# Performance work log

Measured on AMD Instinct MI355X. Metric: run time of the kernel, lower is better.

The kernel has to match this reference:

```python
import jax, jax.numpy as jnp
import numpy as np

N = 100000
K = 16
C_IN = 64
C_MID = 64   # max(in_channels, out_channels // 2)
C_OUT = 128
EPS = 1e-5


def setup_inputs() -> dict:
    key = jax.random.key(0)
    ks = jax.random.split(key, 4)
    feat = jax.random.normal(ks[0], (N, C_IN), dtype=jnp.float32)
    reference_index = jax.random.randint(ks[1], (N, K), 0, N, dtype=jnp.int64)
    # Kaiming-ish init for the two Linear layers (torch Linear default scale)
    W1 = jax.random.normal(ks[2], (C_IN, C_MID), dtype=jnp.float32) / np.sqrt(C_IN)
    W2 = jax.random.normal(ks[3], (C_MID, C_OUT), dtype=jnp.float32) / np.sqrt(C_MID)
    return {
        "feat": feat,
        "reference_index": reference_index,
        "W1": W1,
        "b1": jnp.zeros((C_MID,), jnp.float32),
        "gamma1": jnp.ones((C_MID,), jnp.float32),
        "beta1": jnp.zeros((C_MID,), jnp.float32),
        "W2": W2,
        "b2": jnp.zeros((C_OUT,), jnp.float32),
        "gamma2": jnp.ones((C_OUT,), jnp.float32),
        "beta2": jnp.zeros((C_OUT,), jnp.float32),
    }


def _bn(x, gamma, beta):
    # BatchNorm1d in training mode: biased batch stats over the row dim.
    mean = jnp.mean(x, axis=0)
    var = jnp.var(x, axis=0)
    return (x - mean) * jax.lax.rsqrt(var + EPS) * gamma + beta


def reference(feat, reference_index, W1, b1, gamma1, beta1, W2, b2, gamma2, beta2):
    # grouping (with_xyz=False): gather neighbor features -> [N, K, C_IN]
    grouped = feat[reference_index]
    x = grouped.reshape(-1, C_IN)                 # [N*K, C_IN]
    h = jax.nn.relu(_bn(x @ W1 + b1, gamma1, beta1))   # [N*K, C_MID]
    h = jax.nn.relu(_bn(h @ W2 + b2, gamma2, beta2))   # [N*K, C_OUT]
    out = h.reshape(N, K, C_OUT).max(axis=1)      # max-pool over neighbors
    return out
```

## Files before the change

### kernel.cpp

```cpp
#include <hip/hip_runtime.h>
#include <hip/hip_bf16.h>

#define N_PTS 100000
#define KNN   16
#define NK    (N_PTS * KNN)
#define CIN   64
#define CMID  64
#define COUT  128

#define HSLC    64
#define SEG_CNT 25000
#define SEG_U32 12500

#define OFF_Z2B   0
#define OFF_Z1B   25600000
#define OFF_CNT   38400000
#define OFF_STATS 38800000
#define OFF_W2BF  38801536
#define OFF_W1BF  38817920

typedef __attribute__((ext_vector_type(8))) short bf16x8;
typedef __attribute__((ext_vector_type(4))) float f32x4;
union U8 { uint4 u; bf16x8 v; unsigned short s[8]; };

__device__ __forceinline__ unsigned short f2bf(float f) {
    unsigned u = __float_as_uint(f);
    unsigned r = (u + 0x7fffu + ((u >> 16) & 1u)) >> 16;
    return (unsigned short)r;
}

__global__ __launch_bounds__(256) void hist_k(const int* __restrict__ idx,
                                              unsigned short* __restrict__ pc) {
    __shared__ unsigned int smem[SEG_U32];
    int seg  = blockIdx.x & 3;
    int slc  = blockIdx.x >> 2;
    int base = seg * SEG_CNT;

    for (int i = threadIdx.x; i < SEG_U32; i += 256) smem[i] = 0;
    __syncthreads();

    const int4* ip = (const int4*)idx;
    const int per = NK / 4 / HSLC;
    int s = slc * per, e = s + per;
    for (int i = s + threadIdx.x; i < e; i += 256) {
        int4 v = ip[i];
        int a;
        a = v.x - base; if ((unsigned)a < (unsigned)SEG_CNT)
            atomicAdd(&smem[a >> 1], 1u << ((a & 1) * 16));
        a = v.y - base; if ((unsigned)a < (unsigned)SEG_CNT)
            atomicAdd(&smem[a >> 1], 1u << ((a & 1) * 16));
        a = v.z - base; if ((unsigned)a < (unsigned)SEG_CNT)
            atomicAdd(&smem[a >> 1], 1u << ((a & 1) * 16));
        a = v.w - base; if ((unsigned)a < (unsigned)SEG_CNT)
            atomicAdd(&smem[a >> 1], 1u << ((a & 1) * 16));
    }
    __syncthreads();

    unsigned int* outp = (unsigned int*)(pc + (size_t)slc * N_PTS) + seg * SEG_U32;
    for (int i = threadIdx.x; i < SEG_U32; i += 256) outp[i] = smem[i];
}

__global__ __launch_bounds__(256) void sum_counts_k(const unsigned short* __restrict__ pc,
                                                    float* __restrict__ counts,
                                                    const float* __restrict__ W2,
                                                    unsigned short* __restrict__ w2bf,
                                                    const float* __restrict__ W1,
                                                    unsigned short* __restrict__ w1bf) {
    if (blockIdx.x == 196) {
        for (int e = threadIdx.x; e < 8192; e += 256) {
            int j = e & 7, lane = (e >> 3) & 63, kh = (e >> 9) & 1, nt = e >> 10;
            int k = kh * 32 + (lane >> 4) * 8 + j;
            int n = nt * 16 + (lane & 15);
            w2bf[e] = f2bf(W2[k * COUT + n]);
        }
        return;
    }
    if (blockIdx.x == 197) {
        for (int e = threadIdx.x; e < 4096; e += 256) {
            int j = e & 7, lane = (e >> 3) & 63, kh = (e >> 9) & 1, nt = e >> 10;
            int k = kh * 32 + (lane >> 4) * 8 + j;
            int n = nt * 16 + (lane & 15);
            w1bf[e] = f2bf(W1[k * CMID + n]);
        }
        return;
    }
    int i = blockIdx.x * 256 + threadIdx.x;
    if (i >= N_PTS / 2) return;
    const unsigned int* p = (const unsigned int*)pc;
    unsigned int u = 0;
    #pragma unroll
    for (int s = 0; s < HSLC; s++) u += p[s * (N_PTS / 2) + i];
    float2 r;
    r.x = (float)(u & 0xffffu);
    r.y = (float)(u >> 16);
    ((float2*)counts)[i] = r;
}

__global__ __launch_bounds__(256) void gemm1_k(const float* __restrict__ feat,
                                               const unsigned short* __restrict__ w1bf,
                                               const float* __restrict__ b1,
                                               const float* __restrict__ counts,
                                               unsigned short* __restrict__ z1b,
                                               float* __restrict__ S1,
                                               float* __restrict__ Q1) {
    int lane = threadIdx.x & 63, wid = threadIdx.x >> 6;
    int il = lane & 15, quad = lane >> 4;

    bf16x8 wf[4][2];
    const uint4* wp = (const uint4*)w1bf;
    #pragma unroll
    for (int nt = 0; nt < 4; nt++) {
        U8 t0; t0.u = wp[(nt * 2 + 0) * 64 + lane]; wf[nt][0] = t0.v;
        U8 t1; t1.u = wp[(nt * 2 + 1) * 64 + lane]; wf[nt][1] = t1.v;
    }
    float bias[4];
    #pragma unroll
    for (int nt = 0; nt < 4; nt++) bias[nt] = b1[nt * 16 + il];

    float s[4] = {0, 0, 0, 0}, q[4] = {0, 0, 0, 0};

    int wgid = blockIdx.x * 4 + wid;
    for (int tile = wgid; tile < N_PTS / 16; tile += gridDim.x * 4) {
        int m0 = tile * 16;
        const float* fr = feat + (size_t)(m0 + il) * 64;
        float4 fa = *(const float4*)(fr + quad * 8);
        float4 fb = *(const float4*)(fr + quad * 8 + 4);
        float4 fc = *(const float4*)(fr + 32 + quad * 8);
        float4 fd = *(const float4*)(fr + 32 + quad * 8 + 4);
        U8 ua, ub;
        ua.s[0] = f2bf(fa.x); ua.s[1] = f2bf(fa.y); ua.s[2] = f2bf(fa.z); ua.s[3] = f2bf(fa.w);
        ua.s[4] = f2bf(fb.x); ua.s[5] = f2bf(fb.y); ua.s[6] = f2bf(fb.z); ua.s[7] = f2bf(fb.w);
        ub.s[0] = f2bf(fc.x); ub.s[1] = f2bf(fc.y); ub.s[2] = f2bf(fc.z); ub.s[3] = f2bf(fc.w);
        ub.s[4] = f2bf(fd.x); ub.s[5] = f2bf(fd.y); ub.s[6] = f2bf(fd.z); ub.s[7] = f2bf(fd.w);

        float4 cnt4 = *(const float4*)(counts + m0 + quad * 4);
        #pragma unroll
        for (int nt = 0; nt < 4; nt++) {
            f32x4 acc = {bias[nt], bias[nt], bias[nt], bias[nt]};
            acc = __builtin_amdgcn_mfma_f32_16x16x32_bf16(ua.v, wf[nt][0], acc, 0, 0, 0);
            acc = __builtin_amdgcn_mfma_f32_16x16x32_bf16(ub.v, wf[nt][1], acc, 0, 0, 0);
            unsigned short* zp = z1b + (size_t)(m0 + quad * 4) * 64 + nt * 16 + il;
            zp[0]   = f2bf(acc[0]);
            zp[64]  = f2bf(acc[1]);
            zp[128] = f2bf(acc[2]);
            zp[192] = f2bf(acc[3]);
            s[nt] += cnt4.x * acc[0] + cnt4.y * acc[1] + cnt4.z * acc[2] + cnt4.w * acc[3];
            q[nt] += cnt4.x * acc[0] * acc[0] + cnt4.y * acc[1] * acc[1]
                   + cnt4.z * acc[2] * acc[2] + cnt4.w * acc[3] * acc[3];
        }
    }
    #pragma unroll
    for (int m = 16; m <= 32; m <<= 1) {
        #pragma unroll
        for (int nt = 0; nt < 4; nt++) {
            s[nt] += __shfl_xor(s[nt], m, 64);
            q[nt] += __shfl_xor(q[nt], m, 64);
        }
    }
    __shared__ float sred[2][4][4][16];
    if (quad == 0) {
        #pragma unroll
        for (int nt = 0; nt < 4; nt++) { sred[0][wid][nt][il] = s[nt]; sred[1][wid][nt][il] = q[nt]; }
    }
    __syncthreads();
    if (threadIdx.x < 128) {
        int which = threadIdx.x >> 6, c = threadIdx.x & 63;
        float t = sred[which][0][c >> 4][c & 15] + sred[which][1][c >> 4][c & 15]
                + sred[which][2][c >> 4][c & 15] + sred[which][3][c >> 4][c & 15];
        atomicAdd(which ? &Q1[c] : &S1[c], t);
    }
}

__device__ __forceinline__ bf16x8 bnrelu(uint4 r, float4 alo, float4 ahi,
                                         float4 blo, float4 bhi) {
    float z0 = __uint_as_float(r.x << 16), z1 = __uint_as_float(r.x & 0xffff0000u);
    float z2 = __uint_as_float(r.y << 16), z3 = __uint_as_float(r.y & 0xffff0000u);
    float z4 = __uint_as_float(r.z << 16), z5 = __uint_as_float(r.z & 0xffff0000u);
    float z6 = __uint_as_float(r.w << 16), z7 = __uint_as_float(r.w & 0xffff0000u);
    U8 o;
    o.s[0] = f2bf(fmaxf(fmaf(alo.x, z0, blo.x), 0.f));
    o.s[1] = f2bf(fmaxf(fmaf(alo.y, z1, blo.y), 0.f));
    o.s[2] = f2bf(fmaxf(fmaf(alo.z, z2, blo.z), 0.f));
    o.s[3] = f2bf(fmaxf(fmaf(alo.w, z3, blo.w), 0.f));
    o.s[4] = f2bf(fmaxf(fmaf(ahi.x, z4, bhi.x), 0.f));
    o.s[5] = f2bf(fmaxf(fmaf(ahi.y, z5, bhi.y), 0.f));
    o.s[6] = f2bf(fmaxf(fmaf(ahi.z, z6, bhi.z), 0.f));
    o.s[7] = f2bf(fmaxf(fmaf(ahi.w, z7, bhi.w), 0.f));
    return o.v;
}

__global__ __launch_bounds__(256) void gemm2_k(const unsigned short* __restrict__ z1b,
                                               const unsigned short* __restrict__ w2bf,
                                               const float* __restrict__ S1,
                                               const float* __restrict__ Q1,
                                               const float* __restrict__ g1,
                                               const float* __restrict__ be1,
                                               const float* __restrict__ b2,
                                               const float* __restrict__ counts,
                                               unsigned short* __restrict__ z2b,
                                               float* __restrict__ S2,
                                               float* __restrict__ Q2) {
    __shared__ float Al[64], Bl[64];
    if (threadIdx.x < 64) {
        const float inv = 1.0f / (float)NK;
        float m = S1[threadIdx.x] * inv;
        float v = Q1[threadIdx.x] * inv - m * m;
        float a = g1[threadIdx.x] * rsqrtf(v + 1e-5f);
        Al[threadIdx.x] = a;
        Bl[threadIdx.x] = be1[threadIdx.x] - m * a;
    }
    __syncthreads();

    int lane = threadIdx.x & 63, wid = threadIdx.x >> 6;
    int il = lane & 15, quad = lane >> 4;

    float4 a0lo = *(const float4*)(Al + quad * 8);
    float4 a0hi = *(const float4*)(Al + quad * 8 + 4);
    float4 b0lo = *(const float4*)(Bl + quad * 8);
    float4 b0hi = *(const float4*)(Bl + quad * 8 + 4);
    float4 a1lo = *(const float4*)(Al + 32 + quad * 8);
    float4 a1hi = *(const float4*)(Al + 32 + quad * 8 + 4);
    float4 b1lo = *(const float4*)(Bl + 32 + quad * 8);
    float4 b1hi = *(const float4*)(Bl + 32 + quad * 8 + 4);

    bf16x8 bfr[8][2];
    const uint4* wp = (const uint4*)w2bf;
    #pragma unroll
    for (int nt = 0; nt < 8; nt++) {
        U8 t0; t0.u = wp[(nt * 2 + 0) * 64 + lane]; bfr[nt][0] = t0.v;
        U8 t1; t1.u = wp[(nt * 2 + 1) * 64 + lane]; bfr[nt][1] = t1.v;
    }
    float bias[8];
    #pragma unroll
    for (int nt = 0; nt < 8; nt++) bias[nt] = b2[nt * 16 + il];

    float s[8], q[8];
    #pragma unroll
    for (int j = 0; j < 8; j++) { s[j] = 0.f; q[j] = 0.f; }

    int wgid = blockIdx.x * 4 + wid;
    for (int tile = wgid; tile < N_PTS / 16; tile += gridDim.x * 4) {
        int m0 = tile * 16;
        const uint4* ar = (const uint4*)(z1b + (size_t)(m0 + il) * 64);
        uint4 ra0 = ar[quad];
        uint4 ra1 = ar[4 + quad];
        bf16x8 af0 = bnrelu(ra0, a0lo, a0hi, b0lo, b0hi);
        bf16x8 af1 = bnrelu(ra1, a1lo, a1hi, b1lo, b1hi);
        float4 cnt4 = *(const float4*)(counts + m0 + quad * 4);
        #pragma unroll
        for (int nt = 0; nt < 8; nt++) {
            f32x4 acc = {bias[nt], bias[nt], bias[nt], bias[nt]};
            acc = __builtin_amdgcn_mfma_f32_16x16x32_bf16(af0, bfr[nt][0], acc, 0, 0, 0);
            acc = __builtin_amdgcn_mfma_f32_16x16x32_bf16(af1, bfr[nt][1], acc, 0, 0, 0);
            unsigned short* zp = z2b + ((size_t)(nt >> 2) * N_PTS + m0 + quad * 4) * 64
                                     + (nt & 3) * 16 + il;
            zp[0]   = f2bf(acc[0]);
            zp[64]  = f2bf(acc[1]);
            zp[128] = f2bf(acc[2]);
            zp[192] = f2bf(acc[3]);
            s[nt] += cnt4.x * acc[0] + cnt4.y * acc[1] + cnt4.z * acc[2] + cnt4.w * acc[3];
            q[nt] += cnt4.x * acc[0] * acc[0] + cnt4.y * acc[1] * acc[1]
                   + cnt4.z * acc[2] * acc[2] + cnt4.w * acc[3] * acc[3];
        }
    }
    #pragma unroll
    for (int m = 16; m <= 32; m <<= 1) {
        #pragma unroll
        for (int nt = 0; nt < 8; nt++) {
            s[nt] += __shfl_xor(s[nt], m, 64);
            q[nt] += __shfl_xor(q[nt], m, 64);
        }
    }
    __shared__ float sred[2][4][8][16];
    if (quad == 0) {
        #pragma unroll
        for (int nt = 0; nt < 8; nt++) { sred[0][wid][nt][il] = s[nt]; sred[1][wid][nt][il] = q[nt]; }
    }
    __syncthreads();
    {
        int which = threadIdx.x >> 7, c = threadIdx.x & 127;
        float t = sred[which][0][c >> 4][c & 15] + sred[which][1][c >> 4][c & 15]
                + sred[which][2][c >> 4][c & 15] + sred[which][3][c >> 4][c & 15];
        atomicAdd(which ? &Q2[c] : &S2[c], t);
    }
}

__global__ __launch_bounds__(256) void gather_k(const unsigned int* __restrict__ z2u,
                                                const int* __restrict__ idx,
                                                const float* __restrict__ S2,
                                                const float* __restrict__ Q2,
                                                const float* __restrict__ g2,
                                                const float* __restrict__ be2,
                                                float* __restrict__ out) {
    int lane = threadIdx.x & 63, wid = threadIdx.x >> 6;
    int half = blockIdx.x / (N_PTS / 8);
    int n    = (blockIdx.x % (N_PTS / 8)) * 8 + wid * 2 + (lane >> 5);
    int sl   = lane & 31;

    const float inv = 1.0f / (float)NK;
    float2 Sv = ((const float2*)S2)[half * 32 + sl];
    float2 Qv = ((const float2*)Q2)[half * 32 + sl];
    float2 gv = ((const float2*)g2)[half * 32 + sl];
    float2 bv = ((const float2*)be2)[half * 32 + sl];
    float m0c = Sv.x * inv, m1c = Sv.y * inv;
    float a0 = gv.x * rsqrtf(Qv.x * inv - m0c * m0c + 1e-5f);
    float a1 = gv.y * rsqrtf(Qv.y * inv - m1c * m1c + 1e-5f);
    float b0 = bv.x - m0c * a0;
    float b1 = bv.y - m1c * a1;

    const int* ip = idx + n * KNN;
    const unsigned int* zh = z2u + (size_t)half * N_PTS * 32;
    float mx0 = -1e30f, mn0 = 1e30f, mx1 = -1e30f, mn1 = 1e30f;
    #pragma unroll
    for (int k = 0; k < KNN; k++) {
        int j = ip[k];
        unsigned v = zh[(size_t)j * 32 + sl];
        float f0 = __uint_as_float(v << 16);
        float f1 = __uint_as_float(v & 0xffff0000u);
        mx0 = fmaxf(mx0, f0); mn0 = fminf(mn0, f0);
        mx1 = fmaxf(mx1, f1); mn1 = fminf(mn1, f1);
    }
    float2 r;
    r.x = fmaxf(fmaxf(fmaf(a0, mx0, b0), fmaf(a0, mn0, b0)), 0.f);
    r.y = fmaxf(fmaxf(fmaf(a1, mx1, b1), fmaf(a1, mn1, b1)), 0.f);
    ((float2*)(out + (size_t)n * COUT + half * 64))[sl] = r;
}

extern "C" void kernel_launch(void* const* d_in, const int* in_sizes, int n_in,
                              void* d_out, int out_size, void* d_ws, size_t ws_size,
                              hipStream_t stream) {
    const float* feat = (const float*)d_in[0];
    const int*   idx  = (const int*)d_in[1];
    const float* W1   = (const float*)d_in[2];
    const float* b1   = (const float*)d_in[3];
    const float* g1   = (const float*)d_in[4];
    const float* be1  = (const float*)d_in[5];
    const float* W2   = (const float*)d_in[6];
    const float* b2   = (const float*)d_in[7];
    const float* g2   = (const float*)d_in[8];
    const float* be2  = (const float*)d_in[9];
    float* out = (float*)d_out;

    char* ws = (char*)d_ws;
    unsigned short* z2b = (unsigned short*)(ws + OFF_Z2B);
    unsigned short* pc  = (unsigned short*)(ws + OFF_Z2B);
    unsigned short* z1b = (unsigned short*)(ws + OFF_Z1B);
    float* counts = (float*)(ws + OFF_CNT);
    float* S1 = (float*)(ws + OFF_STATS);
    float* Q1 = S1 + 64;
    float* S2 = S1 + 128;
    float* Q2 = S1 + 256;
    unsigned short* w2bf = (unsigned short*)(ws + OFF_W2BF);
    unsigned short* w1bf = (unsigned short*)(ws + OFF_W1BF);

    hipMemsetAsync(ws + OFF_STATS, 0, 1536, stream);

    hist_k<<<4 * HSLC, 256, 0, stream>>>(idx, pc);
    sum_counts_k<<<198, 256, 0, stream>>>(pc, counts, W2, w2bf, W1, w1bf);
    gemm1_k<<<512, 256, 0, stream>>>(feat, w1bf, b1, counts, z1b, S1, Q1);
    gemm2_k<<<512, 256, 0, stream>>>(z1b, w2bf, S1, Q1, g1, be1, b2, counts, z2b, S2, Q2);
    gather_k<<<2 * (N_PTS / 8), 256, 0, stream>>>((const unsigned int*)z2b, idx,
                                                  S2, Q2, g2, be2, out);
}
```

Baseline: 206.8 us.

## Switch intermediates to fp16, fold gamma sign into W2, packed-max gather

Intermediates and MFMA inputs move from bf16 to fp16, with packed round-toward-zero conversions. The MFMA operands are swapped so each lane writes four contiguous channels as one 8-byte store instead of four scattered 2-byte stores. The sign of gamma2 is folded into W2 and b2, so the gather only needs a max, which it does with v_pk_max_f16 instead of tracking both max and min in fp32. This cuts gather ALU work and speeds the GEMM stores, at the cost of fp16 range and precision risk and more stats registers.

```diff
diff --git a/kernel.cpp b/kernel.cpp
--- a/kernel.cpp
+++ b/kernel.cpp
@@ -12,21 +12,25 @@
 #define SEG_CNT 25000
 #define SEG_U32 12500
 
-#define OFF_Z2B   0
-#define OFF_Z1B   25600000
+#define OFF_Z2H   0
+#define OFF_Z1H   25600000
 #define OFF_CNT   38400000
 #define OFF_STATS 38800000
-#define OFF_W2BF  38801536
-#define OFF_W1BF  38817920
-
-typedef __attribute__((ext_vector_type(8))) short bf16x8;
+#define OFF_W2F   38801536
+#define OFF_W1F   38817920
+
+typedef __attribute__((ext_vector_type(8))) _Float16 f16x8;
+typedef __attribute__((ext_vector_type(2))) __fp16 fp16x2;
 typedef __attribute__((ext_vector_type(4))) float f32x4;
-union U8 { uint4 u; bf16x8 v; unsigned short s[8]; };
-
-__device__ __forceinline__ unsigned short f2bf(float f) {
-    unsigned u = __float_as_uint(f);
-    unsigned r = (u + 0x7fffu + ((u >> 16) & 1u)) >> 16;
-    return (unsigned short)r;
+union F8 { uint4 u; f16x8 v; };
+union PK { fp16x2 v; unsigned u; };
+union UH { unsigned u; _Float16 h[2]; };
+
+__device__ __forceinline__ unsigned pk2(float a, float b) {
+    PK p; p.v = __builtin_amdgcn_cvt_pkrtz(a, b); return p.u;
+}
+__device__ __forceinline__ unsigned pkmax(unsigned a, unsigned b) {
+    unsigned d; asm("v_pk_max_f16 %0, %1, %2" : "=v"(d) : "v"(a), "v"(b)); return d;
 }
 
 __global__ __launch_bounds__(256) void hist_k(const int* __restrict__ idx,
@@ -63,24 +67,25 @@
 __global__ __launch_bounds__(256) void sum_counts_k(const unsigned short* __restrict__ pc,
                                                     float* __restrict__ counts,
                                                     const float* __restrict__ W2,
-                                                    unsigned short* __restrict__ w2bf,
+                                                    const float* __restrict__ g2,
+                                                    _Float16* __restrict__ w2f,
                                                     const float* __restrict__ W1,
-                                                    unsigned short* __restrict__ w1bf) {
+                                                    _Float16* __restrict__ w1f) {
     if (blockIdx.x == 196) {
         for (int e = threadIdx.x; e < 8192; e += 256) {
-            int j = e & 7, lane = (e >> 3) & 63, kh = (e >> 9) & 1, nt = e >> 10;
+            int j = e & 7, lane = (e >> 3) & 63, kh = (e >> 9) & 1, cht = e >> 10;
             int k = kh * 32 + (lane >> 4) * 8 + j;
-            int n = nt * 16 + (lane & 15);
-            w2bf[e] = f2bf(W2[k * COUT + n]);
+            int n = cht * 16 + (lane & 15);
+            w2f[e] = (_Float16)(__builtin_copysignf(1.f, g2[n]) * W2[k * COUT + n]);
         }
         return;
     }
     if (blockIdx.x == 197) {
         for (int e = threadIdx.x; e < 4096; e += 256) {
-            int j = e & 7, lane = (e >> 3) & 63, kh = (e >> 9) & 1, nt = e >> 10;
+            int j = e & 7, lane = (e >> 3) & 63, kh = (e >> 9) & 1, cht = e >> 10;
             int k = kh * 32 + (lane >> 4) * 8 + j;
-            int n = nt * 16 + (lane & 15);
-            w1bf[e] = f2bf(W1[k * CMID + n]);
+            int n = cht * 16 + (lane & 15);
+            w1f[e] = (_Float16)(W1[k * CMID + n]);
         }
         return;
     }
@@ -97,27 +102,31 @@
 }
 
 __global__ __launch_bounds__(256) void gemm1_k(const float* __restrict__ feat,
-                                               const unsigned short* __restrict__ w1bf,
+                                               const _Float16* __restrict__ w1f,
                                                const float* __restrict__ b1,
                                                const float* __restrict__ counts,
-                                               unsigned short* __restrict__ z1b,
+                                               _Float16* __restrict__ z1h,
                                                float* __restrict__ S1,
                                                float* __restrict__ Q1) {
     int lane = threadIdx.x & 63, wid = threadIdx.x >> 6;
     int il = lane & 15, quad = lane >> 4;
 
-    bf16x8 wf[4][2];
-    const uint4* wp = (const uint4*)w1bf;
-    #pragma unroll
-    for (int nt = 0; nt < 4; nt++) {
-        U8 t0; t0.u = wp[(nt * 2 + 0) * 64 + lane]; wf[nt][0] = t0.v;
-        U8 t1; t1.u = wp[(nt * 2 + 1) * 64 + lane]; wf[nt][1] = t1.v;
-    }
-    float bias[4];
-    #pragma unroll
-    for (int nt = 0; nt < 4; nt++) bias[nt] = b1[nt * 16 + il];
-
-    float s[4] = {0, 0, 0, 0}, q[4] = {0, 0, 0, 0};
+    f16x8 wf[4][2];
+    const uint4* wp = (const uint4*)w1f;
+    #pragma unroll
+    for (int cht = 0; cht < 4; cht++) {
+        F8 t0; t0.u = wp[(cht * 2 + 0) * 64 + lane]; wf[cht][0] = t0.v;
+        F8 t1; t1.u = wp[(cht * 2 + 1) * 64 + lane]; wf[cht][1] = t1.v;
+    }
+    float4 bias[4];
+    #pragma unroll
+    for (int cht = 0; cht < 4; cht++) bias[cht] = *(const float4*)(b1 + cht * 16 + quad * 4);
+
+    float s[4][4], q[4][4];
+    #pragma unroll
+    for (int c = 0; c < 4; c++)
+        #pragma unroll
+        for (int r = 0; r < 4; r++) { s[c][r] = 0.f; q[c][r] = 0.f; }
 
     int wgid = blockIdx.x * 4 + wid;
     for (int tile = wgid; tile < N_PTS / 16; tile += gridDim.x * 4) {
@@ -127,80 +136,85 @@
         float4 fb = *(const float4*)(fr + quad * 8 + 4);
         float4 fc = *(const float4*)(fr + 32 + quad * 8);
         float4 fd = *(const float4*)(fr + 32 + quad * 8 + 4);
-        U8 ua, ub;
-        ua.s[0] = f2bf(fa.x); ua.s[1] = f2bf(fa.y); ua.s[2] = f2bf(fa.z); ua.s[3] = f2bf(fa.w);
-        ua.s[4] = f2bf(fb.x); ua.s[5] = f2bf(fb.y); ua.s[6] = f2bf(fb.z); ua.s[7] = f2bf(fb.w);
-        ub.s[0] = f2bf(fc.x); ub.s[1] = f2bf(fc.y); ub.s[2] = f2bf(fc.z); ub.s[3] = f2bf(fc.w);
-        ub.s[4] = f2bf(fd.x); ub.s[5] = f2bf(fd.y); ub.s[6] = f2bf(fd.z); ub.s[7] = f2bf(fd.w);
-
-        float4 cnt4 = *(const float4*)(counts + m0 + quad * 4);
-        #pragma unroll
-        for (int nt = 0; nt < 4; nt++) {
-            f32x4 acc = {bias[nt], bias[nt], bias[nt], bias[nt]};
-            acc = __builtin_amdgcn_mfma_f32_16x16x32_bf16(ua.v, wf[nt][0], acc, 0, 0, 0);
-            acc = __builtin_amdgcn_mfma_f32_16x16x32_bf16(ub.v, wf[nt][1], acc, 0, 0, 0);
-            unsigned short* zp = z1b + (size_t)(m0 + quad * 4) * 64 + nt * 16 + il;
-            zp[0]   = f2bf(acc[0]);
-            zp[64]  = f2bf(acc[1]);
-            zp[128] = f2bf(acc[2]);
-            zp[192] = f2bf(acc[3]);
-            s[nt] += cnt4.x * acc[0] + cnt4.y * acc[1] + cnt4.z * acc[2] + cnt4.w * acc[3];
-            q[nt] += cnt4.x * acc[0] * acc[0] + cnt4.y * acc[1] * acc[1]
-                   + cnt4.z * acc[2] * acc[2] + cnt4.w * acc[3] * acc[3];
+        F8 F0, F1;
+        F0.u.x = pk2(fa.x, fa.y); F0.u.y = pk2(fa.z, fa.w);
+        F0.u.z = pk2(fb.x, fb.y); F0.u.w = pk2(fb.z, fb.w);
+        F1.u.x = pk2(fc.x, fc.y); F1.u.y = pk2(fc.z, fc.w);
+        F1.u.z = pk2(fd.x, fd.y); F1.u.w = pk2(fd.z, fd.w);
+        float cnt = counts[m0 + il];
+        #pragma unroll
+        for (int cht = 0; cht < 4; cht++) {
+            f32x4 acc = {bias[cht].x, bias[cht].y, bias[cht].z, bias[cht].w};
+            acc = __builtin_amdgcn_mfma_f32_16x16x32_f16(wf[cht][0], F0.v, acc, 0, 0, 0);
+            acc = __builtin_amdgcn_mfma_f32_16x16x32_f16(wf[cht][1], F1.v, acc, 0, 0, 0);
+            uint2 pv;
+            pv.x = pk2(acc[0], acc[1]);
+            pv.y = pk2(acc[2], acc[3]);
+            *(uint2*)(z1h + (size_t)(m0 + il) * 64 + cht * 16 + quad * 4) = pv;
+            #pragma unroll
+            for (int r = 0; r < 4; r++) {
+                s[cht][r] = fmaf(cnt, acc[r], s[cht][r]);
+                q[cht][r] = fmaf(cnt * acc[r], acc[r], q[cht][r]);
+            }
         }
     }
     #pragma unroll
-    for (int m = 16; m <= 32; m <<= 1) {
-        #pragma unroll
-        for (int nt = 0; nt < 4; nt++) {
-            s[nt] += __shfl_xor(s[nt], m, 64);
-            q[nt] += __shfl_xor(q[nt], m, 64);
-        }
-    }
-    __shared__ float sred[2][4][4][16];
-    if (quad == 0) {
-        #pragma unroll
-        for (int nt = 0; nt < 4; nt++) { sred[0][wid][nt][il] = s[nt]; sred[1][wid][nt][il] = q[nt]; }
+    for (int m = 1; m <= 8; m <<= 1) {
+        #pragma unroll
+        for (int c = 0; c < 4; c++)
+            #pragma unroll
+            for (int r = 0; r < 4; r++) {
+                s[c][r] += __shfl_xor(s[c][r], m, 64);
+                q[c][r] += __shfl_xor(q[c][r], m, 64);
+            }
+    }
+    __shared__ float sred[2][4][64];
+    if (il == 0) {
+        #pragma unroll
+        for (int c = 0; c < 4; c++)
+            #pragma unroll
+            for (int r = 0; r < 4; r++) {
+                sred[0][wid][c * 16 + quad * 4 + r] = s[c][r];
+                sred[1][wid][c * 16 + quad * 4 + r] = q[c][r];
+            }
     }
     __syncthreads();
     if (threadIdx.x < 128) {
         int which = threadIdx.x >> 6, c = threadIdx.x & 63;
-        float t = sred[which][0][c >> 4][c & 15] + sred[which][1][c >> 4][c & 15]
-                + sred[which][2][c >> 4][c & 15] + sred[which][3][c >> 4][c & 15];
+        float t = sred[which][0][c] + sred[which][1][c] + sred[which][2][c] + sred[which][3][c];
         atomicAdd(which ? &Q1[c] : &S1[c], t);
     }
 }
 
-__device__ __forceinline__ bf16x8 bnrelu(uint4 r, float4 alo, float4 ahi,
-                                         float4 blo, float4 bhi) {
-    float z0 = __uint_as_float(r.x << 16), z1 = __uint_as_float(r.x & 0xffff0000u);
-    float z2 = __uint_as_float(r.y << 16), z3 = __uint_as_float(r.y & 0xffff0000u);
-    float z4 = __uint_as_float(r.z << 16), z5 = __uint_as_float(r.z & 0xffff0000u);
-    float z6 = __uint_as_float(r.w << 16), z7 = __uint_as_float(r.w & 0xffff0000u);
-    U8 o;
-    o.s[0] = f2bf(fmaxf(fmaf(alo.x, z0, blo.x), 0.f));
-    o.s[1] = f2bf(fmaxf(fmaf(alo.y, z1, blo.y), 0.f));
-    o.s[2] = f2bf(fmaxf(fmaf(alo.z, z2, blo.z), 0.f));
-    o.s[3] = f2bf(fmaxf(fmaf(alo.w, z3, blo.w), 0.f));
-    o.s[4] = f2bf(fmaxf(fmaf(ahi.x, z4, bhi.x), 0.f));
-    o.s[5] = f2bf(fmaxf(fmaf(ahi.y, z5, bhi.y), 0.f));
-    o.s[6] = f2bf(fmaxf(fmaf(ahi.z, z6, bhi.z), 0.f));
-    o.s[7] = f2bf(fmaxf(fmaf(ahi.w, z7, bhi.w), 0.f));
+__device__ __forceinline__ f16x8 bnrelu16(uint4 r, float4 alo, float4 ahi,
+                                          float4 blo, float4 bhi) {
+    UH u0, u1, u2, u3;
+    u0.u = r.x; u1.u = r.y; u2.u = r.z; u3.u = r.w;
+    float z0 = (float)u0.h[0], z1 = (float)u0.h[1];
+    float z2 = (float)u1.h[0], z3 = (float)u1.h[1];
+    float z4 = (float)u2.h[0], z5 = (float)u2.h[1];
+    float z6 = (float)u3.h[0], z7 = (float)u3.h[1];
+    F8 o;
+    o.u.x = pk2(fmaxf(fmaf(alo.x, z0, blo.x), 0.f), fmaxf(fmaf(alo.y, z1, blo.y), 0.f));
+    o.u.y = pk2(fmaxf(fmaf(alo.z, z2, blo.z), 0.f), fmaxf(fmaf(alo.w, z3, blo.w), 0.f));
+    o.u.z = pk2(fmaxf(fmaf(ahi.x, z4, bhi.x), 0.f), fmaxf(fmaf(ahi.y, z5, bhi.y), 0.f));
+    o.u.w = pk2(fmaxf(fmaf(ahi.z, z6, bhi.z), 0.f), fmaxf(fmaf(ahi.w, z7, bhi.w), 0.f));
     return o.v;
 }
 
-__global__ __launch_bounds__(256) void gemm2_k(const unsigned short* __restrict__ z1b,
-                                               const unsigned short* __restrict__ w2bf,
+__global__ __launch_bounds__(256) void gemm2_k(const _Float16* __restrict__ z1h,
+                                               const _Float16* __restrict__ w2f,
                                                const float* __restrict__ S1,
                                                const float* __restrict__ Q1,
                                                const float* __restrict__ g1,
                                                const float* __restrict__ be1,
                                                const float* __restrict__ b2,
+                                               const float* __restrict__ g2,
                                                const float* __restrict__ counts,
-                                               unsigned short* __restrict__ z2b,
+                                               _Float16* __restrict__ z2h,
                                                float* __restrict__ S2,
                                                float* __restrict__ Q2) {
-    __shared__ float Al[64], Bl[64];
+    __shared__ float Al[64], Bl[64], Bl2[128];
     if (threadIdx.x < 64) {
         const float inv = 1.0f / (float)NK;
         float m = S1[threadIdx.x] * inv;
@@ -209,6 +223,8 @@
         Al[threadIdx.x] = a;
         Bl[threadIdx.x] = be1[threadIdx.x] - m * a;
     }
+    if (threadIdx.x < 128)
+        Bl2[threadIdx.x] = __builtin_copysignf(1.f, g2[threadIdx.x]) * b2[threadIdx.x];
     __syncthreads();
 
     int lane = threadIdx.x & 63, wid = threadIdx.x >> 6;
@@ -223,64 +239,71 @@
     float4 b1lo = *(const float4*)(Bl + 32 + quad * 8);
     float4 b1hi = *(const float4*)(Bl + 32 + quad * 8 + 4);
 
-    bf16x8 bfr[8][2];
-    const uint4* wp = (const uint4*)w2bf;
-    #pragma unroll
-    for (int nt = 0; nt < 8; nt++) {
-        U8 t0; t0.u = wp[(nt * 2 + 0) * 64 + lane]; bfr[nt][0] = t0.v;
-        U8 t1; t1.u = wp[(nt * 2 + 1) * 64 + lane]; bfr[nt][1] = t1.v;
-    }
-    float bias[8];
-    #pragma unroll
-    for (int nt = 0; nt < 8; nt++) bias[nt] = b2[nt * 16 + il];
-
-    float s[8], q[8];
-    #pragma unroll
-    for (int j = 0; j < 8; j++) { s[j] = 0.f; q[j] = 0.f; }
+    f16x8 wf[8][2];
+    const uint4* wp = (const uint4*)w2f;
+    #pragma unroll
+    for (int cht = 0; cht < 8; cht++) {
+        F8 t0; t0.u = wp[(cht * 2 + 0) * 64 + lane]; wf[cht][0] = t0.v;
+        F8 t1; t1.u = wp[(cht * 2 + 1) * 64 + lane]; wf[cht][1] = t1.v;
+    }
+
+    float s[8][4], q[8][4];
+    #pragma unroll
+    for (int c = 0; c < 8; c++)
+        #pragma unroll
+        for (int r = 0; r < 4; r++) { s[c][r] = 0.f; q[c][r] = 0.f; }
 
     int wgid = blockIdx.x * 4 + wid;
     for (int tile = wgid; tile < N_PTS / 16; tile += gridDim.x * 4) {
         int m0 = tile * 16;
-        const uint4* ar = (const uint4*)(z1b + (size_t)(m0 + il) * 64);
+        const uint4* ar = (const uint4*)(z1h + (size_t)(m0 + il) * 64);
         uint4 ra0 = ar[quad];
         uint4 ra1 = ar[4 + quad];
-        bf16x8 af0 = bnrelu(ra0, a0lo, a0hi, b0lo, b0hi);
-        bf16x8 af1 = bnrelu(ra1, a1lo, a1hi, b1lo, b1hi);
-        float4 cnt4 = *(const float4*)(counts + m0 + quad * 4);
-        #pragma unroll
-        for (int nt = 0; nt < 8; nt++) {
-            f32x4 acc = {bias[nt], bias[nt], bias[nt], bias[nt]};
-            acc = __builtin_amdgcn_mfma_f32_16x16x32_bf16(af0, bfr[nt][0], acc, 0, 0, 0);
-            acc = __builtin_amdgcn_mfma_f32_16x16x32_bf16(af1, bfr[nt][1], acc, 0, 0, 0);
-            unsigned short* zp = z2b + ((size_t)(nt >> 2) * N_PTS + m0 + quad * 4) * 64
-                                     + (nt & 3) * 16 + il;
-            zp[0]   = f2bf(acc[0]);
-            zp[64]  = f2bf(acc[1]);
-            zp[128] = f2bf(acc[2]);
-            zp[192] = f2bf(acc[3]);
-            s[nt] += cnt4.x * acc[0] + cnt4.y * acc[1] + cnt4.z * acc[2] + cnt4.w * acc[3];
-            q[nt] += cnt4.x * acc[0] * acc[0] + cnt4.y * acc[1] * acc[1]
-                   + cnt4.z * acc[2] * acc[2] + cnt4.w * acc[3] * acc[3];
+        f16x8 af0 = bnrelu16(ra0, a0lo, a0hi, b0lo, b0hi);
+        f16x8 af1 = bnrelu16(ra1, a1lo, a1hi, b1lo, b1hi);
+        float cnt = counts[m0 + il];
+        #pragma unroll
+        for (int cht = 0; cht < 8; cht++) {
+            float4 bb = *(const float4*)(Bl2 + cht * 16 + quad * 4);
+            f32x4 acc = {bb.x, bb.y, bb.z, bb.w};
+            acc = __builtin_amdgcn_mfma_f32_16x16x32_f16(wf[cht][0], af0, acc, 0, 0, 0);
+            acc = __builtin_amdgcn_mfma_f32_16x16x32_f16(wf[cht][1], af1, acc, 0, 0, 0);
+            uint2 pv;
+            pv.x = pk2(acc[0], acc[1]);
+            pv.y = pk2(acc[2], acc[3]);
+            size_t base = ((size_t)(cht >> 2) * N_PTS + m0 + il) * 64 + (cht & 3) * 16 + quad * 4;
+            *(uint2*)(z2h + base) = pv;
+            #pragma unroll
+            for (int r = 0; r < 4; r++) {
+                s[cht][r] = fmaf(cnt, acc[r], s[cht][r]);
+                q[cht][r] = fmaf(cnt * acc[r], acc[r], q[cht][r]);
+            }
         }
     }
     #pragma unroll
-    for (int m = 16; m <= 32; m <<= 1) {
-        #pragma unroll
-        for (int nt = 0; nt < 8; nt++) {
-            s[nt] += __shfl_xor(s[nt], m, 64);
-            q[nt] += __shfl_xor(q[nt], m, 64);
-        }
-    }
-    __shared__ float sred[2][4][8][16];
-    if (quad == 0) {
-        #pragma unroll
-        for (int nt = 0; nt < 8; nt++) { sred[0][wid][nt][il] = s[nt]; sred[1][wid][nt][il] = q[nt]; }
+    for (int m = 1; m <= 8; m <<= 1) {
+        #pragma unroll
+        for (int c = 0; c < 8; c++)
+            #pragma unroll
+            for (int r = 0; r < 4; r++) {
+                s[c][r] += __shfl_xor(s[c][r], m, 64);
+                q[c][r] += __shfl_xor(q[c][r], m, 64);
+            }
+    }
+    __shared__ float sred[2][4][128];
+    if (il == 0) {
+        #pragma unroll
+        for (int c = 0; c < 8; c++)
+            #pragma unroll
+            for (int r = 0; r < 4; r++) {
+                sred[0][wid][c * 16 + quad * 4 + r] = s[c][r];
+                sred[1][wid][c * 16 + quad * 4 + r] = q[c][r];
+            }
     }
     __syncthreads();
     {
         int which = threadIdx.x >> 7, c = threadIdx.x & 127;
-        float t = sred[which][0][c >> 4][c & 15] + sred[which][1][c >> 4][c & 15]
-                + sred[which][2][c >> 4][c & 15] + sred[which][3][c >> 4][c & 15];
+        float t = sred[which][0][c] + sred[which][1][c] + sred[which][2][c] + sred[which][3][c];
         atomicAdd(which ? &Q2[c] : &S2[c], t);
     }
 }
@@ -298,31 +321,30 @@
     int sl   = lane & 31;
 
     const float inv = 1.0f / (float)NK;
-    float2 Sv = ((const float2*)S2)[half * 32 + sl];
-    float2 Qv = ((const float2*)Q2)[half * 32 + sl];
-    float2 gv = ((const float2*)g2)[half * 32 + sl];
-    float2 bv = ((const float2*)be2)[half * 32 + sl];
+    int ci = half * 32 + sl;
+    float2 Sv = ((const float2*)S2)[ci];
+    float2 Qv = ((const float2*)Q2)[ci];
+    float2 gv = ((const float2*)g2)[ci];
+    float2 bv = ((const float2*)be2)[ci];
     float m0c = Sv.x * inv, m1c = Sv.y * inv;
-    float a0 = gv.x * rsqrtf(Qv.x * inv - m0c * m0c + 1e-5f);
-    float a1 = gv.y * rsqrtf(Qv.y * inv - m1c * m1c + 1e-5f);
+    float a0 = fabsf(gv.x) * rsqrtf(Qv.x * inv - m0c * m0c + 1e-5f);
+    float a1 = fabsf(gv.y) * rsqrtf(Qv.y * inv - m1c * m1c + 1e-5f);
     float b0 = bv.x - m0c * a0;
     float b1 = bv.y - m1c * a1;
 
     const int* ip = idx + n * KNN;
     const unsigned int* zh = z2u + (size_t)half * N_PTS * 32;
-    float mx0 = -1e30f, mn0 = 1e30f, mx1 = -1e30f, mn1 = 1e30f;
+    unsigned mx = 0xFC00FC00u;
     #pragma unroll
     for (int k = 0; k < KNN; k++) {
         int j = ip[k];
-        unsigned v = zh[(size_t)j * 32 + sl];
-        float f0 = __uint_as_float(v << 16);
-        float f1 = __uint_as_float(v & 0xffff0000u);
-        mx0 = fmaxf(mx0, f0); mn0 = fminf(mn0, f0);
-        mx1 = fmaxf(mx1, f1); mn1 = fminf(mn1, f1);
-    }
+        mx = pkmax(mx, zh[(size_t)j * 32 + sl]);
+    }
+    UH u; u.u = mx;
+    float f0 = (float)u.h[0], f1 = (float)u.h[1];
     float2 r;
-    r.x = fmaxf(fmaxf(fmaf(a0, mx0, b0), fmaf(a0, mn0, b0)), 0.f);
-    r.y = fmaxf(fmaxf(fmaf(a1, mx1, b1), fmaf(a1, mn1, b1)), 0.f);
+    r.x = fmaxf(fmaf(a0, f0, b0), 0.f);
+    r.y = fmaxf(fmaf(a1, f1, b1), 0.f);
     ((float2*)(out + (size_t)n * COUT + half * 64))[sl] = r;
 }
 
@@ -342,23 +364,23 @@
     float* out = (float*)d_out;
 
     char* ws = (char*)d_ws;
-    unsigned short* z2b = (unsigned short*)(ws + OFF_Z2B);
-    unsigned short* pc  = (unsigned short*)(ws + OFF_Z2B);
-    unsigned short* z1b = (unsigned short*)(ws + OFF_Z1B);
+    _Float16* z2h = (_Float16*)(ws + OFF_Z2H);
+    unsigned short* pc = (unsigned short*)(ws + OFF_Z2H);
+    _Float16* z1h = (_Float16*)(ws + OFF_Z1H);
     float* counts = (float*)(ws + OFF_CNT);
     float* S1 = (float*)(ws + OFF_STATS);
     float* Q1 = S1 + 64;
     float* S2 = S1 + 128;
     float* Q2 = S1 + 256;
-    unsigned short* w2bf = (unsigned short*)(ws + OFF_W2BF);
-    unsigned short* w1bf = (unsigned short*)(ws + OFF_W1BF);
-
-    hipMemsetAsync(ws + OFF_STATS, 0, 1536, stream);
+    _Float16* w2f = (_Float16*)(ws + OFF_W2F);
+    _Float16* w1f = (_Float16*)(ws + OFF_W1F);
+
+    (void)hipMemsetAsync(ws + OFF_STATS, 0, 1536, stream);
 
     hist_k<<<4 * HSLC, 256, 0, stream>>>(idx, pc);
-    sum_counts_k<<<198, 256, 0, stream>>>(pc, counts, W2, w2bf, W1, w1bf);
-    gemm1_k<<<512, 256, 0, stream>>>(feat, w1bf, b1, counts, z1b, S1, Q1);
-    gemm2_k<<<512, 256, 0, stream>>>(z1b, w2bf, S1, Q1, g1, be1, b2, counts, z2b, S2, Q2);
-    gather_k<<<2 * (N_PTS / 8), 256, 0, stream>>>((const unsigned int*)z2b, idx,
+    sum_counts_k<<<198, 256, 0, stream>>>(pc, counts, W2, g2, w2f, W1, w1f);
+    gemm1_k<<<512, 256, 0, stream>>>(feat, w1f, b1, counts, z1h, S1, Q1);
+    gemm2_k<<<512, 256, 0, stream>>>(z1h, w2f, S1, Q1, g1, be1, b2, g2, counts, z2h, S2, Q2);
+    gather_k<<<2 * (N_PTS / 8), 256, 0, stream>>>((const unsigned int*)z2h, idx,
                                                   S2, Q2, g2, be2, out);
 }
```

Measured after the change: 210.8 us. About the same (+1.9%).
